# Kernel optimization log

Measured on AMD Instinct MI355X. Metric: run time of the kernel, lower is better.

The kernel has to match this reference:

```python
import jax, jax.numpy as jnp
import numpy as np

NUM_NODES = 10000
NUM_EDGES = 640000
GNN_IN = 128
EDGE_DIST_DIM = 4
MLP_HIDDEN = 256
MLP_OUT = 1


def setup_inputs() -> dict:
    key = jax.random.key(0)
    k1, k2, k3, k4, k5 = jax.random.split(key, 5)
    x = jax.random.normal(k1, (NUM_NODES, GNN_IN), dtype=jnp.float32)
    edge_index = jax.random.randint(k2, (NUM_EDGES, 2), 0, NUM_NODES, dtype=jnp.int64)
    edge_dist = jax.random.normal(k3, (NUM_EDGES, EDGE_DIST_DIM), dtype=jnp.float32)
    d_in = GNN_IN * 2 + EDGE_DIST_DIM
    # Kaiming-uniform-ish init like nn.Linear defaults
    w1 = jax.random.uniform(k4, (d_in, MLP_HIDDEN), dtype=jnp.float32,
                            minval=-1.0, maxval=1.0) / np.sqrt(d_in)
    b1 = jnp.zeros((MLP_HIDDEN,), dtype=jnp.float32)
    w2 = jax.random.uniform(k5, (MLP_HIDDEN, MLP_OUT), dtype=jnp.float32,
                            minval=-1.0, maxval=1.0) / np.sqrt(MLP_HIDDEN)
    b2 = jnp.zeros((MLP_OUT,), dtype=jnp.float32)
    return {"x": x, "edge_index": edge_index, "edge_dist": edge_dist,
            "w1": w1, "b1": b1, "w2": w2, "b2": b2}


def reference(x, edge_index, edge_dist, w1, b1, w2, b2):
    # edge_index: (num_edges, 2) -> transpose to (2, num_edges) as in forward()
    row = edge_index[:, 0]
    col = edge_index[:, 1]
    # gather node features for both endpoints, concat with edge distances
    edge_attr = jnp.concatenate([x[row], x[col], edge_dist], axis=1)  # (E, 2*gnn_in+edge_dist_dim)
    h = jax.nn.relu(edge_attr @ w1 + b1)  # (E, mlp_hidden)
    return jax.nn.sigmoid(h @ w2 + b2)    # (E, mlp_out)
```

## Files before the change

### kernel.cpp

```cpp
#include <hip/hip_runtime.h>
#include <hip/hip_fp16.h>

#define GNN_IN 128
#define HID 256
#define NSPLIT 4
#define SLICE 64

typedef _Float16 f16x2 __attribute__((ext_vector_type(2)));
struct __align__(8) h4v { f16x2 a, b; };
struct __align__(16) h8v { f16x2 a, b, c, d; };

__device__ __forceinline__ float fdot2f(f16x2 a, f16x2 b, float c) {
#if __has_builtin(__builtin_amdgcn_fdot2)
    return __builtin_amdgcn_fdot2(a, b, c, false);
#else
    return fmaf((float)a.x, (float)b.x, fmaf((float)a.y, (float)b.y, c));
#endif
}

__device__ __forceinline__ f16x2 pkcvt(float x, float y) {
#if __has_builtin(__builtin_amdgcn_cvt_pkrtz)
    return __builtin_bit_cast(f16x2, __builtin_amdgcn_cvt_pkrtz(x, y));
#else
    f16x2 r; r.x = (_Float16)x; r.y = (_Float16)y; return r;
#endif
}

#define DPP_ADD(v, ctrl)                                                     \
    do {                                                                     \
        float _t = __builtin_bit_cast(                                       \
            float, __builtin_amdgcn_update_dpp(                              \
                       0, __builtin_bit_cast(int, v), ctrl, 0xf, 0xf, true));\
        (v) += _t;                                                           \
    } while (0)

__device__ __forceinline__ float dpp_sum8(float v) {
    DPP_ADD(v, 0x111);
    DPP_ADD(v, 0x112);
    DPP_ADD(v, 0x114);
    return v;
}

__device__ __forceinline__ float dpp_sum64(float v) {
    DPP_ADD(v, 0x111);
    DPP_ADD(v, 0x112);
    DPP_ADD(v, 0x114);
    DPP_ADD(v, 0x118);
    DPP_ADD(v, 0x142);
    DPP_ADD(v, 0x143);
    return v;
}

__global__ void detect_kernel(const unsigned int* __restrict__ ei,
                              unsigned int* __restrict__ flag) {
    if (threadIdx.x == 0 && blockIdx.x == 0) {
        unsigned int v = 0;
        for (int i = 1; i < 256; i += 2) v |= ei[i];
        *flag = (v == 0u) ? 1u : 0u;
    }
}

__global__ void __launch_bounds__(256) decode_kernel(
    const void* __restrict__ ei, const unsigned int* __restrict__ flag,
    int2* __restrict__ idx, int ne) {
    const int e = blockIdx.x * 256 + threadIdx.x;
    if (e >= ne) return;
    if (*flag) {
        const int4 v = *(const int4*)((const char*)ei + (size_t)e * 16);
        idx[e] = make_int2(v.x, v.z);
    } else {
        idx[e] = ((const int2*)ei)[e];
    }
}

__global__ void __launch_bounds__(256) node_gemm_c4(
    const float* __restrict__ x, const float* __restrict__ w1,
    __half* __restrict__ AB, int num_nodes) {
    __shared__ float xs[16][GNN_IN];
    const int tid = threadIdx.x;
    const int r0  = blockIdx.x * 16;

    for (int i = tid; i < 16 * GNN_IN / 4; i += 256) {
        const int rr = i >> 5;
        const int cc = (i & 31) << 2;
        const int r = min(r0 + rr, num_nodes - 1);
        *(float4*)&xs[rr][cc] = *(const float4*)(x + (size_t)r * GNN_IN + cc);
    }
    __syncthreads();

    const int cq   = tid & 127;
    const int rg   = tid >> 7;
    const int col  = (cq & 63) << 2;
    const int half = cq >> 6;
    const float* __restrict__ w = w1 + (size_t)half * GNN_IN * HID + col;

    float acc[8][4];
#pragma unroll
    for (int r = 0; r < 8; ++r)
#pragma unroll
        for (int c = 0; c < 4; ++c) acc[r][c] = 0.f;

    for (int k0 = 0; k0 < GNN_IN; k0 += 4) {
        float4 wv[4];
#pragma unroll
        for (int kk = 0; kk < 4; ++kk)
            wv[kk] = *(const float4*)(w + (size_t)(k0 + kk) * HID);
#pragma unroll
        for (int r = 0; r < 8; ++r) {
            const float4 xv = *(const float4*)&xs[rg * 8 + r][k0];
            acc[r][0] = fmaf(xv.x, wv[0].x, acc[r][0]);
            acc[r][1] = fmaf(xv.x, wv[0].y, acc[r][1]);
            acc[r][2] = fmaf(xv.x, wv[0].z, acc[r][2]);
            acc[r][3] = fmaf(xv.x, wv[0].w, acc[r][3]);
            acc[r][0] = fmaf(xv.y, wv[1].x, acc[r][0]);
            acc[r][1] = fmaf(xv.y, wv[1].y, acc[r][1]);
            acc[r][2] = fmaf(xv.y, wv[1].z, acc[r][2]);
            acc[r][3] = fmaf(xv.y, wv[1].w, acc[r][3]);
            acc[r][0] = fmaf(xv.z, wv[2].x, acc[r][0]);
            acc[r][1] = fmaf(xv.z, wv[2].y, acc[r][1]);
            acc[r][2] = fmaf(xv.z, wv[2].z, acc[r][2]);
            acc[r][3] = fmaf(xv.z, wv[2].w, acc[r][3]);
            acc[r][0] = fmaf(xv.w, wv[3].x, acc[r][0]);
            acc[r][1] = fmaf(xv.w, wv[3].y, acc[r][1]);
            acc[r][2] = fmaf(xv.w, wv[3].z, acc[r][2]);
            acc[r][3] = fmaf(xv.w, wv[3].w, acc[r][3]);
        }
    }

    __half* o = AB + (size_t)half * num_nodes * HID + col;
#pragma unroll
    for (int r = 0; r < 8; ++r) {
        const int rr = r0 + rg * 8 + r;
        if (rr < num_nodes) {
            h4v hv;
            hv.a = pkcvt(acc[r][0], acc[r][1]);
            hv.b = pkcvt(acc[r][2], acc[r][3]);
            *(h4v*)(o + (size_t)rr * HID) = hv;
        }
    }
}

__global__ void __launch_bounds__(256) edge_split_kernel(
    const __half* __restrict__ AB, const int2* __restrict__ idx,
    const float* __restrict__ ed, const float* __restrict__ w1,
    const float* __restrict__ b1, const float* __restrict__ w2,
    float* __restrict__ partials, int num_edges, int num_nodes) {
    const int tid   = threadIdx.x;
    const int lane  = tid & 63;
    const int bid   = blockIdx.x;
    const int split = (bid & 7) >> 1;
    const int wsi   = ((((bid >> 3) << 1) | (bid & 1)) << 2) | (tid >> 6);
    const int nsw   = (gridDim.x >> 3) << 3;
    const int j8    = lane >> 3;
    const int q8    = lane & 7;
    const int c     = split * SLICE + (q8 << 3);

    f16x2 wtA[8], wtB[8], w2pk[4];
    float b1f[8];
#pragma unroll
    for (int cc = 0; cc < 8; ++cc) {
        wtA[cc] = pkcvt(w1[(size_t)(2 * GNN_IN + 0) * HID + c + cc],
                        w1[(size_t)(2 * GNN_IN + 1) * HID + c + cc]);
        wtB[cc] = pkcvt(w1[(size_t)(2 * GNN_IN + 2) * HID + c + cc],
                        w1[(size_t)(2 * GNN_IN + 3) * HID + c + cc]);
        b1f[cc] = b1[c + cc];
    }
#pragma unroll
    for (int m = 0; m < 4; ++m)
        w2pk[m] = pkcvt(w2[c + 2 * m], w2[c + 2 * m + 1]);
    const f16x2 zero = {(_Float16)0.f, (_Float16)0.f};

    const __half* __restrict__ A = AB;
    const __half* __restrict__ B = AB + (size_t)num_nodes * HID;
    float* __restrict__ pbase = partials + (size_t)split * num_edges;
    const int ngroups = (num_edges + 7) >> 3;

    for (int g0 = wsi; g0 < ngroups; g0 += 2 * nsw) {
        const int g1 = min(g0 + nsw, ngroups - 1);
        const int e0 = min(g0 * 8 + j8, num_edges - 1);
        const int e1 = min(g1 * 8 + j8, num_edges - 1);

        const int2  rc0 = idx[e0];
        const int2  rc1 = idx[e1];
        const float4 edv0 = *(const float4*)(ed + (size_t)e0 * 4);
        const float4 edv1 = *(const float4*)(ed + (size_t)e1 * 4);
        const h8v av0 = *(const h8v*)(A + (size_t)rc0.x * HID + c);
        const h8v bv0 = *(const h8v*)(B + (size_t)rc0.y * HID + c);
        const h8v av1 = *(const h8v*)(A + (size_t)rc1.x * HID + c);
        const h8v bv1 = *(const h8v*)(B + (size_t)rc1.y * HID + c);

        float p0, p1;
        {
            const f16x2 e01 = pkcvt(edv0.x, edv0.y);
            const f16x2 e23 = pkcvt(edv0.z, edv0.w);
            float c_[8];
#pragma unroll
            for (int cc = 0; cc < 8; ++cc)
                c_[cc] = fdot2f(e23, wtB[cc], fdot2f(e01, wtA[cc], b1f[cc]));
            f16x2 h0 = (av0.a + bv0.a) + pkcvt(c_[0], c_[1]);
            f16x2 h1 = (av0.b + bv0.b) + pkcvt(c_[2], c_[3]);
            f16x2 h2 = (av0.c + bv0.c) + pkcvt(c_[4], c_[5]);
            f16x2 h3 = (av0.d + bv0.d) + pkcvt(c_[6], c_[7]);
            h0 = __builtin_elementwise_max(h0, zero);
            h1 = __builtin_elementwise_max(h1, zero);
            h2 = __builtin_elementwise_max(h2, zero);
            h3 = __builtin_elementwise_max(h3, zero);
            p0 = fdot2f(h0, w2pk[0],
                 fdot2f(h1, w2pk[1], fdot2f(h2, w2pk[2], fdot2f(h3, w2pk[3], 0.f))));
        }
        {
            const f16x2 e01 = pkcvt(edv1.x, edv1.y);
            const f16x2 e23 = pkcvt(edv1.z, edv1.w);
            float c_[8];
#pragma unroll
            for (int cc = 0; cc < 8; ++cc)
                c_[cc] = fdot2f(e23, wtB[cc], fdot2f(e01, wtA[cc], b1f[cc]));
            f16x2 h0 = (av1.a + bv1.a) + pkcvt(c_[0], c_[1]);
            f16x2 h1 = (av1.b + bv1.b) + pkcvt(c_[2], c_[3]);
            f16x2 h2 = (av1.c + bv1.c) + pkcvt(c_[4], c_[5]);
            f16x2 h3 = (av1.d + bv1.d) + pkcvt(c_[6], c_[7]);
            h0 = __builtin_elementwise_max(h0, zero);
            h1 = __builtin_elementwise_max(h1, zero);
            h2 = __builtin_elementwise_max(h2, zero);
            h3 = __builtin_elementwise_max(h3, zero);
            p1 = fdot2f(h0, w2pk[0],
                 fdot2f(h1, w2pk[1], fdot2f(h2, w2pk[2], fdot2f(h3, w2pk[3], 0.f))));
        }

        p0 = dpp_sum8(p0);
        p1 = dpp_sum8(p1);
        if (q8 == 7) {
            pbase[e0] = p0;
            if (g1 != g0) pbase[e1] = p1;
        }
    }
}

__global__ void __launch_bounds__(256) combine_kernel(
    const float* __restrict__ partials, const float* __restrict__ b2,
    float* __restrict__ out, int ne) {
    const int e0 = (blockIdx.x * 256 + threadIdx.x) * 4;
    if (e0 >= ne) return;
    const float b2v = b2[0];
    if (e0 + 3 < ne) {
        float4 s0 = *(const float4*)(partials + e0);
        const float4 s1 = *(const float4*)(partials + (size_t)ne + e0);
        const float4 s2 = *(const float4*)(partials + (size_t)2 * ne + e0);
        const float4 s3 = *(const float4*)(partials + (size_t)3 * ne + e0);
        s0.x = 1.f / (1.f + __expf(-(s0.x + s1.x + s2.x + s3.x + b2v)));
        s0.y = 1.f / (1.f + __expf(-(s0.y + s1.y + s2.y + s3.y + b2v)));
        s0.z = 1.f / (1.f + __expf(-(s0.z + s1.z + s2.z + s3.z + b2v)));
        s0.w = 1.f / (1.f + __expf(-(s0.w + s1.w + s2.w + s3.w + b2v)));
        *(float4*)(out + e0) = s0;
    } else {
        for (int e = e0; e < ne; ++e) {
            const float p = partials[e] + partials[(size_t)ne + e] +
                            partials[(size_t)2 * ne + e] +
                            partials[(size_t)3 * ne + e];
            out[e] = 1.f / (1.f + __expf(-(p + b2v)));
        }
    }
}

__global__ void __launch_bounds__(256) edge_kernel_fp16(
    const __half* __restrict__ A, const __half* __restrict__ B,
    const void* __restrict__ ei, const float* __restrict__ ed,
    const float* __restrict__ w1, const float* __restrict__ b1,
    const float* __restrict__ w2, const float* __restrict__ b2,
    const unsigned int* __restrict__ flag,
    float* __restrict__ out, int num_edges) {
    const int lane   = threadIdx.x & 63;
    const int wave   = (blockIdx.x * blockDim.x + threadIdx.x) >> 6;
    const int nwaves = (gridDim.x * blockDim.x) >> 6;
    const int c0     = lane << 2;

    const float4 b1v = *(const float4*)(b1 + c0);
    float wt[4][4];
#pragma unroll
    for (int k = 0; k < 4; ++k)
        *(float4*)wt[k] = *(const float4*)(w1 + (size_t)(2 * GNN_IN + k) * HID + c0);
    const float4 w2f = *(const float4*)(w2 + c0);
    const f16x2  w2A = pkcvt(w2f.x, w2f.y);
    const f16x2  w2B = pkcvt(w2f.z, w2f.w);
    const float  b2v = b2[0];
    const int   is64 = __builtin_amdgcn_readfirstlane((int)(*flag));
    const f16x2 zero = {(_Float16)0.f, (_Float16)0.f};

    const int chunk = (((num_edges + nwaves - 1) / nwaves) + 3) & ~3;
    const int e0s = __builtin_amdgcn_readfirstlane(wave * chunk);
    const int e1s = __builtin_amdgcn_readfirstlane(min(num_edges, e0s + chunk));

    for (int es = e0s; es < e1s; es += 4) {
        int eid[4];
#pragma unroll
        for (int jj = 0; jj < 4; ++jj) eid[jj] = min(es + jj, e1s - 1);
        int rr[4], cc[4];
        if (is64) {
#pragma unroll
            for (int jj = 0; jj < 4; ++jj) {
                const int4 v = *(const int4*)((const char*)ei + (size_t)eid[jj] * 16);
                rr[jj] = v.x; cc[jj] = v.z;
            }
        } else {
#pragma unroll
            for (int jj = 0; jj < 4; ++jj) {
                const int2 v = *(const int2*)((const char*)ei + (size_t)eid[jj] * 8);
                rr[jj] = v.x; cc[jj] = v.y;
            }
        }
        h4v av[4], bv[4];
        float4 edv[4];
#pragma unroll
        for (int jj = 0; jj < 4; ++jj) {
            av[jj]  = *(const h4v*)(A + (size_t)rr[jj] * HID + c0);
            bv[jj]  = *(const h4v*)(B + (size_t)cc[jj] * HID + c0);
            edv[jj] = *(const float4*)(ed + (size_t)eid[jj] * 4);
        }
        float p[4];
#pragma unroll
        for (int jj = 0; jj < 4; ++jj) {
            float c_[4] = {b1v.x, b1v.y, b1v.z, b1v.w};
            const float ep[4] = {edv[jj].x, edv[jj].y, edv[jj].z, edv[jj].w};
#pragma unroll
            for (int k = 0; k < 4; ++k)
#pragma unroll
                for (int qq = 0; qq < 4; ++qq) c_[qq] = fmaf(ep[k], wt[k][qq], c_[qq]);
            f16x2 h0 = (av[jj].a + bv[jj].a) + pkcvt(c_[0], c_[1]);
            f16x2 h1 = (av[jj].b + bv[jj].b) + pkcvt(c_[2], c_[3]);
            h0 = __builtin_elementwise_max(h0, zero);
            h1 = __builtin_elementwise_max(h1, zero);
            p[jj] = fdot2f(h0, w2A, fdot2f(h1, w2B, 0.f));
        }
#pragma unroll
        for (int jj = 0; jj < 4; ++jj) p[jj] = dpp_sum64(p[jj]);
        float s[4];
#pragma unroll
        for (int jj = 0; jj < 4; ++jj) s[jj] = 1.f / (1.f + __expf(-(p[jj] + b2v)));
        if (lane == 63) {
            if (es + 3 < e1s) {
                *(float4*)(out + es) = make_float4(s[0], s[1], s[2], s[3]);
            } else {
#pragma unroll
                for (int jj = 0; jj < 4; ++jj)
                    if (es + jj < e1s) out[es + jj] = s[jj];
            }
        }
    }
}

__global__ void __launch_bounds__(256) edge_direct_kernel(
    const float* __restrict__ x, const void* __restrict__ ei,
    const float* __restrict__ ed, const float* __restrict__ w1,
    const float* __restrict__ b1, const float* __restrict__ w2,
    const float* __restrict__ b2, const unsigned int* __restrict__ flag,
    float* __restrict__ out, int num_edges, int num_nodes) {
    const int lane   = threadIdx.x & 63;
    const int wave   = (blockIdx.x * blockDim.x + threadIdx.x) >> 6;
    const int nwaves = (gridDim.x * blockDim.x) >> 6;
    const int c0     = lane << 2;

    const float4 w2v = *(const float4*)(w2 + c0);
    const float4 b1v = *(const float4*)(b1 + c0);
    float wt[4][4];
#pragma unroll
    for (int k = 0; k < 4; ++k)
        *(float4*)wt[k] = *(const float4*)(w1 + (size_t)(2 * GNN_IN + k) * HID + c0);
    const float b2v  = b2[0];
    const int   is64 = flag ? (int)(*flag) : 0;
    const float* w2p = (const float*)&w2v;
    const float* b1p = (const float*)&b1v;

    const int chunk = (num_edges + nwaves - 1) / nwaves;
    const int e0 = wave * chunk;
    const int e1 = min(num_edges, e0 + chunk);

    for (int e = e0; e < e1; ++e) {
        int row, col;
        if (is64) {
            const int4 v = ((const int4*)ei)[e];
            row = v.x; col = v.z;
        } else {
            const int2 v = ((const int2*)ei)[e];
            row = v.x; col = v.y;
        }
        row = min(max(row, 0), num_nodes - 1);
        col = min(max(col, 0), num_nodes - 1);
        const float4 edv = *(const float4*)(ed + (size_t)e * 4);
        const float* edp = (const float*)&edv;
        float h4[4];
#pragma unroll
        for (int jj = 0; jj < 4; ++jj) {
            float h = b1p[jj];
#pragma unroll
            for (int k = 0; k < 4; ++k) h = fmaf(edp[k], wt[k][jj], h);
            h4[jj] = h;
        }
        const float* xr = x + (size_t)row * GNN_IN;
        const float* xc = x + (size_t)col * GNN_IN;
        for (int k = 0; k < GNN_IN; ++k) {
            const float xv = xr[k];
            const float4 wv = *(const float4*)(w1 + (size_t)k * HID + c0);
            h4[0] = fmaf(xv, wv.x, h4[0]); h4[1] = fmaf(xv, wv.y, h4[1]);
            h4[2] = fmaf(xv, wv.z, h4[2]); h4[3] = fmaf(xv, wv.w, h4[3]);
        }
        for (int k = 0; k < GNN_IN; ++k) {
            const float xv = xc[k];
            const float4 wv = *(const float4*)(w1 + (size_t)(GNN_IN + k) * HID + c0);
            h4[0] = fmaf(xv, wv.x, h4[0]); h4[1] = fmaf(xv, wv.y, h4[1]);
            h4[2] = fmaf(xv, wv.z, h4[2]); h4[3] = fmaf(xv, wv.w, h4[3]);
        }
        float p = 0.f;
#pragma unroll
        for (int jj = 0; jj < 4; ++jj) p = fmaf(fmaxf(h4[jj], 0.f), w2p[jj], p);
#pragma unroll
        for (int off = 32; off >= 1; off >>= 1) p += __shfl_xor(p, off, 64);
        if (lane == 0) out[e] = 1.f / (1.f + __expf(-(p + b2v)));
    }
}

extern "C" void kernel_launch(void* const* d_in, const int* in_sizes, int n_in,
                              void* d_out, int out_size, void* d_ws, size_t ws_size,
                              hipStream_t stream) {
    const float* x  = (const float*)d_in[0];
    const void*  ei = d_in[1];
    const float* ed = (const float*)d_in[2];
    const float* w1 = (const float*)d_in[3];
    const float* b1 = (const float*)d_in[4];
    const float* w2 = (const float*)d_in[5];
    const float* b2 = (const float*)d_in[6];
    float* out = (float*)d_out;

    const int num_nodes = in_sizes[0] / GNN_IN;
    const int num_edges = in_sizes[1] / 2;

    unsigned int* flag = nullptr;
    if (ws_size >= 16) {
        flag = (unsigned int*)d_ws;
        detect_kernel<<<1, 64, 0, stream>>>((const unsigned int*)ei, flag);
    }

    const size_t ab_bytes   = (size_t)2 * num_nodes * HID * sizeof(__half);
    const size_t idx_bytes  = (size_t)num_edges * sizeof(int2);
    const size_t part_bytes = (size_t)NSPLIT * num_edges * sizeof(float);
    const size_t need_split = 256 + ab_bytes + idx_bytes + part_bytes;
    const size_t need_old   = 256 + ab_bytes;

    if (flag && ws_size >= need_split) {
        __half* AB      = (__half*)((char*)d_ws + 256);
        int2*   idx     = (int2*)((char*)d_ws + 256 + ab_bytes);
        float*  partial = (float*)((char*)d_ws + 256 + ab_bytes + idx_bytes);

        decode_kernel<<<(num_edges + 255) / 256, 256, 0, stream>>>(ei, flag, idx,
                                                                   num_edges);
        node_gemm_c4<<<(num_nodes + 15) / 16, 256, 0, stream>>>(x, w1, AB,
                                                                num_nodes);
        edge_split_kernel<<<2048, 256, 0, stream>>>(AB, idx, ed, w1, b1, w2,
                                                    partial, num_edges, num_nodes);
        combine_kernel<<<(num_edges / 4 + 255) / 256, 256, 0, stream>>>(
            partial, b2, out, num_edges);
    } else if (flag && ws_size >= need_old) {
        __half* AB = (__half*)((char*)d_ws + 256);
        node_gemm_c4<<<(num_nodes + 15) / 16, 256, 0, stream>>>(x, w1, AB,
                                                                num_nodes);
        __half* Bp = AB + (size_t)num_nodes * HID;
        edge_kernel_fp16<<<2048, 256, 0, stream>>>(AB, Bp, ei, ed, w1, b1, w2, b2,
                                                   flag, out, num_edges);
    } else {
        edge_direct_kernel<<<4096, 256, 0, stream>>>(x, ei, ed, w1, b1, w2, b2,
                                                     flag, out, num_edges, num_nodes);
    }
}
```

Measured before the change: 100.6 us.

## Pack edge records with fp16 distances, fp16 node GEMM, and 4-way edge batching

The decode kernel now writes one 16-byte record per edge holding pre-shifted row/col byte offsets and fp16-packed edge distances, so the edge kernel issues a single load instead of separate index and distance loads. The node GEMM converts x and W1 to fp16 in two small prep kernels and uses packed fp16 dot products. The edge kernel processes four edge groups per iteration to keep more gathers in flight, with launch bounds and register pinning added. This adds two extra kernel launches and more workspace, and raises register pressure in the edge loop.

```diff
diff --git a/kernel.cpp b/kernel.cpp
--- a/kernel.cpp
+++ b/kernel.cpp
@@ -25,6 +25,13 @@
     f16x2 r; r.x = (_Float16)x; r.y = (_Float16)y; return r;
 #endif
 }
+
+__device__ __forceinline__ void pinv(f16x2& x) {
+    int t = __builtin_bit_cast(int, x);
+    asm volatile("" : "+v"(t));
+    x = __builtin_bit_cast(f16x2, t);
+}
+__device__ __forceinline__ void pinf(float& x) { asm volatile("" : "+v"(x)); }
 
 #define DPP_ADD(v, ctrl)                                                     \
     do {                                                                     \
@@ -61,30 +68,60 @@
 }
 
 __global__ void __launch_bounds__(256) decode_kernel(
-    const void* __restrict__ ei, const unsigned int* __restrict__ flag,
-    int2* __restrict__ idx, int ne) {
+    const void* __restrict__ ei, const float* __restrict__ ed,
+    const unsigned int* __restrict__ flag, int4* __restrict__ recs, int ne) {
     const int e = blockIdx.x * 256 + threadIdx.x;
     if (e >= ne) return;
+    int r, c;
     if (*flag) {
         const int4 v = *(const int4*)((const char*)ei + (size_t)e * 16);
-        idx[e] = make_int2(v.x, v.z);
+        r = v.x; c = v.z;
     } else {
-        idx[e] = ((const int2*)ei)[e];
-    }
-}
-
-__global__ void __launch_bounds__(256) node_gemm_c4(
-    const float* __restrict__ x, const float* __restrict__ w1,
+        const int2 v = ((const int2*)ei)[e];
+        r = v.x; c = v.y;
+    }
+    const float4 d = *(const float4*)(ed + (size_t)e * 4);
+    int4 rec;
+    rec.x = r << 9;
+    rec.y = c << 9;
+    rec.z = __builtin_bit_cast(int, pkcvt(d.x, d.y));
+    rec.w = __builtin_bit_cast(int, pkcvt(d.z, d.w));
+    recs[e] = rec;
+}
+
+__global__ void __launch_bounds__(256) prep_x_kernel(
+    const float* __restrict__ x, __half* __restrict__ xh, int n4) {
+    const int i = blockIdx.x * 256 + threadIdx.x;
+    if (i >= n4) return;
+    const float4 v = ((const float4*)x)[i];
+    h4v o;
+    o.a = pkcvt(v.x, v.y);
+    o.b = pkcvt(v.z, v.w);
+    ((h4v*)xh)[i] = o;
+}
+
+__global__ void __launch_bounds__(256) prep_w_kernel(
+    const float* __restrict__ w1, f16x2* __restrict__ whp) {
+    const int i = blockIdx.x * 256 + threadIdx.x;
+    if (i >= 2 * 64 * 256) return;
+    const int col  = i & 255;
+    const int p    = (i >> 8) & 63;
+    const int half = i >> 14;
+    const int k    = half * GNN_IN + 2 * p;
+    whp[i] = pkcvt(w1[(size_t)k * HID + col], w1[(size_t)(k + 1) * HID + col]);
+}
+
+__global__ void __launch_bounds__(256) node_gemm_fp16(
+    const __half* __restrict__ xh, const f16x2* __restrict__ whp,
     __half* __restrict__ AB, int num_nodes) {
-    __shared__ float xs[16][GNN_IN];
+    __shared__ __half xs[16][GNN_IN];
     const int tid = threadIdx.x;
     const int r0  = blockIdx.x * 16;
-
-    for (int i = tid; i < 16 * GNN_IN / 4; i += 256) {
-        const int rr = i >> 5;
-        const int cc = (i & 31) << 2;
-        const int r = min(r0 + rr, num_nodes - 1);
-        *(float4*)&xs[rr][cc] = *(const float4*)(x + (size_t)r * GNN_IN + cc);
+    {
+        const int rr = tid >> 4;
+        const int cc = (tid & 15) << 3;
+        const int r  = min(r0 + rr, num_nodes - 1);
+        *(h8v*)&xs[rr][cc] = *(const h8v*)(xh + (size_t)r * GNN_IN + cc);
     }
     __syncthreads();
 
@@ -92,7 +129,7 @@
     const int rg   = tid >> 7;
     const int col  = (cq & 63) << 2;
     const int half = cq >> 6;
-    const float* __restrict__ w = w1 + (size_t)half * GNN_IN * HID + col;
+    const f16x2* __restrict__ wbase = whp + ((size_t)half << 14) + col;
 
     float acc[8][4];
 #pragma unroll
@@ -100,30 +137,30 @@
 #pragma unroll
         for (int c = 0; c < 4; ++c) acc[r][c] = 0.f;
 
-    for (int k0 = 0; k0 < GNN_IN; k0 += 4) {
-        float4 wv[4];
-#pragma unroll
-        for (int kk = 0; kk < 4; ++kk)
-            wv[kk] = *(const float4*)(w + (size_t)(k0 + kk) * HID);
+    for (int ch = 0; ch < 16; ++ch) {
+        h8v wq[4];
+#pragma unroll
+        for (int p = 0; p < 4; ++p)
+            wq[p] = *(const h8v*)(wbase + (size_t)(ch * 4 + p) * HID);
 #pragma unroll
         for (int r = 0; r < 8; ++r) {
-            const float4 xv = *(const float4*)&xs[rg * 8 + r][k0];
-            acc[r][0] = fmaf(xv.x, wv[0].x, acc[r][0]);
-            acc[r][1] = fmaf(xv.x, wv[0].y, acc[r][1]);
-            acc[r][2] = fmaf(xv.x, wv[0].z, acc[r][2]);
-            acc[r][3] = fmaf(xv.x, wv[0].w, acc[r][3]);
-            acc[r][0] = fmaf(xv.y, wv[1].x, acc[r][0]);
-            acc[r][1] = fmaf(xv.y, wv[1].y, acc[r][1]);
-            acc[r][2] = fmaf(xv.y, wv[1].z, acc[r][2]);
-            acc[r][3] = fmaf(xv.y, wv[1].w, acc[r][3]);
-            acc[r][0] = fmaf(xv.z, wv[2].x, acc[r][0]);
-            acc[r][1] = fmaf(xv.z, wv[2].y, acc[r][1]);
-            acc[r][2] = fmaf(xv.z, wv[2].z, acc[r][2]);
-            acc[r][3] = fmaf(xv.z, wv[2].w, acc[r][3]);
-            acc[r][0] = fmaf(xv.w, wv[3].x, acc[r][0]);
-            acc[r][1] = fmaf(xv.w, wv[3].y, acc[r][1]);
-            acc[r][2] = fmaf(xv.w, wv[3].z, acc[r][2]);
-            acc[r][3] = fmaf(xv.w, wv[3].w, acc[r][3]);
+            const h8v xv = *(const h8v*)&xs[rg * 8 + r][ch * 8];
+            acc[r][0] = fdot2f(xv.a, wq[0].a, acc[r][0]);
+            acc[r][0] = fdot2f(xv.b, wq[1].a, acc[r][0]);
+            acc[r][0] = fdot2f(xv.c, wq[2].a, acc[r][0]);
+            acc[r][0] = fdot2f(xv.d, wq[3].a, acc[r][0]);
+            acc[r][1] = fdot2f(xv.a, wq[0].b, acc[r][1]);
+            acc[r][1] = fdot2f(xv.b, wq[1].b, acc[r][1]);
+            acc[r][1] = fdot2f(xv.c, wq[2].b, acc[r][1]);
+            acc[r][1] = fdot2f(xv.d, wq[3].b, acc[r][1]);
+            acc[r][2] = fdot2f(xv.a, wq[0].c, acc[r][2]);
+            acc[r][2] = fdot2f(xv.b, wq[1].c, acc[r][2]);
+            acc[r][2] = fdot2f(xv.c, wq[2].c, acc[r][2]);
+            acc[r][2] = fdot2f(xv.d, wq[3].c, acc[r][2]);
+            acc[r][3] = fdot2f(xv.a, wq[0].d, acc[r][3]);
+            acc[r][3] = fdot2f(xv.b, wq[1].d, acc[r][3]);
+            acc[r][3] = fdot2f(xv.c, wq[2].d, acc[r][3]);
+            acc[r][3] = fdot2f(xv.d, wq[3].d, acc[r][3]);
         }
     }
 
@@ -140,11 +177,11 @@
     }
 }
 
-__global__ void __launch_bounds__(256) edge_split_kernel(
-    const __half* __restrict__ AB, const int2* __restrict__ idx,
-    const float* __restrict__ ed, const float* __restrict__ w1,
-    const float* __restrict__ b1, const float* __restrict__ w2,
-    float* __restrict__ partials, int num_edges, int num_nodes) {
+__global__ void __launch_bounds__(256, 4) edge_split_kernel(
+    const __half* __restrict__ AB, const int4* __restrict__ recs,
+    const float* __restrict__ w1, const float* __restrict__ b1,
+    const float* __restrict__ w2, float* __restrict__ partials,
+    int num_edges, int num_nodes) {
     const int tid   = threadIdx.x;
     const int lane  = tid & 63;
     const int bid   = blockIdx.x;
@@ -154,6 +191,7 @@
     const int j8    = lane >> 3;
     const int q8    = lane & 7;
     const int c     = split * SLICE + (q8 << 3);
+    const int coff  = c * 2;
 
     f16x2 wtA[8], wtB[8], w2pk[4];
     float b1f[8];
@@ -164,74 +202,58 @@
         wtB[cc] = pkcvt(w1[(size_t)(2 * GNN_IN + 2) * HID + c + cc],
                         w1[(size_t)(2 * GNN_IN + 3) * HID + c + cc]);
         b1f[cc] = b1[c + cc];
-    }
-#pragma unroll
-    for (int m = 0; m < 4; ++m)
+        pinv(wtA[cc]); pinv(wtB[cc]); pinf(b1f[cc]);
+    }
+#pragma unroll
+    for (int m = 0; m < 4; ++m) {
         w2pk[m] = pkcvt(w2[c + 2 * m], w2[c + 2 * m + 1]);
+        pinv(w2pk[m]);
+    }
     const f16x2 zero = {(_Float16)0.f, (_Float16)0.f};
 
-    const __half* __restrict__ A = AB;
-    const __half* __restrict__ B = AB + (size_t)num_nodes * HID;
+    const char* __restrict__ Abase = (const char*)AB;
+    const char* __restrict__ Bbase = (const char*)(AB + (size_t)num_nodes * HID);
     float* __restrict__ pbase = partials + (size_t)split * num_edges;
     const int ngroups = (num_edges + 7) >> 3;
-
-    for (int g0 = wsi; g0 < ngroups; g0 += 2 * nsw) {
-        const int g1 = min(g0 + nsw, ngroups - 1);
-        const int e0 = min(g0 * 8 + j8, num_edges - 1);
-        const int e1 = min(g1 * 8 + j8, num_edges - 1);
-
-        const int2  rc0 = idx[e0];
-        const int2  rc1 = idx[e1];
-        const float4 edv0 = *(const float4*)(ed + (size_t)e0 * 4);
-        const float4 edv1 = *(const float4*)(ed + (size_t)e1 * 4);
-        const h8v av0 = *(const h8v*)(A + (size_t)rc0.x * HID + c);
-        const h8v bv0 = *(const h8v*)(B + (size_t)rc0.y * HID + c);
-        const h8v av1 = *(const h8v*)(A + (size_t)rc1.x * HID + c);
-        const h8v bv1 = *(const h8v*)(B + (size_t)rc1.y * HID + c);
-
-        float p0, p1;
-        {
-            const f16x2 e01 = pkcvt(edv0.x, edv0.y);
-            const f16x2 e23 = pkcvt(edv0.z, edv0.w);
+    const int emax = num_edges - 1;
+
+    for (int g = wsi; g < ngroups; g += 4 * nsw) {
+        int e[4];
+        int4 rec[4];
+#pragma unroll
+        for (int k = 0; k < 4; ++k) {
+            int gk = g + k * nsw;
+            if (gk > ngroups - 1) gk = ngroups - 1;
+            e[k] = min(gk * 8 + j8, emax);
+            rec[k] = recs[e[k]];
+        }
+        h8v av[4], bv[4];
+#pragma unroll
+        for (int k = 0; k < 4; ++k) {
+            av[k] = *(const h8v*)(Abase + ((size_t)(unsigned)(rec[k].x + coff)));
+            bv[k] = *(const h8v*)(Bbase + ((size_t)(unsigned)(rec[k].y + coff)));
+        }
+#pragma unroll
+        for (int k = 0; k < 4; ++k) {
+            const f16x2 e01 = __builtin_bit_cast(f16x2, rec[k].z);
+            const f16x2 e23 = __builtin_bit_cast(f16x2, rec[k].w);
             float c_[8];
 #pragma unroll
             for (int cc = 0; cc < 8; ++cc)
                 c_[cc] = fdot2f(e23, wtB[cc], fdot2f(e01, wtA[cc], b1f[cc]));
-            f16x2 h0 = (av0.a + bv0.a) + pkcvt(c_[0], c_[1]);
-            f16x2 h1 = (av0.b + bv0.b) + pkcvt(c_[2], c_[3]);
-            f16x2 h2 = (av0.c + bv0.c) + pkcvt(c_[4], c_[5]);
-            f16x2 h3 = (av0.d + bv0.d) + pkcvt(c_[6], c_[7]);
+            f16x2 h0 = (av[k].a + bv[k].a) + pkcvt(c_[0], c_[1]);
+            f16x2 h1 = (av[k].b + bv[k].b) + pkcvt(c_[2], c_[3]);
+            f16x2 h2 = (av[k].c + bv[k].c) + pkcvt(c_[4], c_[5]);
+            f16x2 h3 = (av[k].d + bv[k].d) + pkcvt(c_[6], c_[7]);
             h0 = __builtin_elementwise_max(h0, zero);
             h1 = __builtin_elementwise_max(h1, zero);
             h2 = __builtin_elementwise_max(h2, zero);
             h3 = __builtin_elementwise_max(h3, zero);
-            p0 = fdot2f(h0, w2pk[0],
-                 fdot2f(h1, w2pk[1], fdot2f(h2, w2pk[2], fdot2f(h3, w2pk[3], 0.f))));
-        }
-        {
-            const f16x2 e01 = pkcvt(edv1.x, edv1.y);
-            const f16x2 e23 = pkcvt(edv1.z, edv1.w);
-            float c_[8];
-#pragma unroll
-            for (int cc = 0; cc < 8; ++cc)
-                c_[cc] = fdot2f(e23, wtB[cc], fdot2f(e01, wtA[cc], b1f[cc]));
-            f16x2 h0 = (av1.a + bv1.a) + pkcvt(c_[0], c_[1]);
-            f16x2 h1 = (av1.b + bv1.b) + pkcvt(c_[2], c_[3]);
-            f16x2 h2 = (av1.c + bv1.c) + pkcvt(c_[4], c_[5]);
-            f16x2 h3 = (av1.d + bv1.d) + pkcvt(c_[6], c_[7]);
-            h0 = __builtin_elementwise_max(h0, zero);
-            h1 = __builtin_elementwise_max(h1, zero);
-            h2 = __builtin_elementwise_max(h2, zero);
-            h3 = __builtin_elementwise_max(h3, zero);
-            p1 = fdot2f(h0, w2pk[0],
-                 fdot2f(h1, w2pk[1], fdot2f(h2, w2pk[2], fdot2f(h3, w2pk[3], 0.f))));
-        }
-
-        p0 = dpp_sum8(p0);
-        p1 = dpp_sum8(p1);
-        if (q8 == 7) {
-            pbase[e0] = p0;
-            if (g1 != g0) pbase[e1] = p1;
+            float p = fdot2f(h0, w2pk[0],
+                      fdot2f(h1, w2pk[1],
+                      fdot2f(h2, w2pk[2], fdot2f(h3, w2pk[3], 0.f))));
+            p = dpp_sum8(p);
+            if (q8 == 7) pbase[e[k]] = p;
         }
     }
 }
@@ -262,6 +284,68 @@
     }
 }
 
+__global__ void __launch_bounds__(256) node_gemm_c4(
+    const float* __restrict__ x, const float* __restrict__ w1,
+    __half* __restrict__ AB, int num_nodes) {
+    __shared__ float xs[16][GNN_IN];
+    const int tid = threadIdx.x;
+    const int r0  = blockIdx.x * 16;
+    for (int i = tid; i < 16 * GNN_IN / 4; i += 256) {
+        const int rr = i >> 5;
+        const int cc = (i & 31) << 2;
+        const int r = min(r0 + rr, num_nodes - 1);
+        *(float4*)&xs[rr][cc] = *(const float4*)(x + (size_t)r * GNN_IN + cc);
+    }
+    __syncthreads();
+    const int cq   = tid & 127;
+    const int rg   = tid >> 7;
+    const int col  = (cq & 63) << 2;
+    const int half = cq >> 6;
+    const float* __restrict__ w = w1 + (size_t)half * GNN_IN * HID + col;
+    float acc[8][4];
+#pragma unroll
+    for (int r = 0; r < 8; ++r)
+#pragma unroll
+        for (int c = 0; c < 4; ++c) acc[r][c] = 0.f;
+    for (int k0 = 0; k0 < GNN_IN; k0 += 4) {
+        float4 wv[4];
+#pragma unroll
+        for (int kk = 0; kk < 4; ++kk)
+            wv[kk] = *(const float4*)(w + (size_t)(k0 + kk) * HID);
+#pragma unroll
+        for (int r = 0; r < 8; ++r) {
+            const float4 xv = *(const float4*)&xs[rg * 8 + r][k0];
+            acc[r][0] = fmaf(xv.x, wv[0].x, acc[r][0]);
+            acc[r][1] = fmaf(xv.x, wv[0].y, acc[r][1]);
+            acc[r][2] = fmaf(xv.x, wv[0].z, acc[r][2]);
+            acc[r][3] = fmaf(xv.x, wv[0].w, acc[r][3]);
+            acc[r][0] = fmaf(xv.y, wv[1].x, acc[r][0]);
+            acc[r][1] = fmaf(xv.y, wv[1].y, acc[r][1]);
+            acc[r][2] = fmaf(xv.y, wv[1].z, acc[r][2]);
+            acc[r][3] = fmaf(xv.y, wv[1].w, acc[r][3]);
+            acc[r][0] = fmaf(xv.z, wv[2].x, acc[r][0]);
+            acc[r][1] = fmaf(xv.z, wv[2].y, acc[r][1]);
+            acc[r][2] = fmaf(xv.z, wv[2].z, acc[r][2]);
+            acc[r][3] = fmaf(xv.z, wv[2].w, acc[r][3]);
+            acc[r][0] = fmaf(xv.w, wv[3].x, acc[r][0]);
+            acc[r][1] = fmaf(xv.w, wv[3].y, acc[r][1]);
+            acc[r][2] = fmaf(xv.w, wv[3].z, acc[r][2]);
+            acc[r][3] = fmaf(xv.w, wv[3].w, acc[r][3]);
+        }
+    }
+    __half* o = AB + (size_t)half * num_nodes * HID + col;
+#pragma unroll
+    for (int r = 0; r < 8; ++r) {
+        const int rr = r0 + rg * 8 + r;
+        if (rr < num_nodes) {
+            h4v hv;
+            hv.a = pkcvt(acc[r][0], acc[r][1]);
+            hv.b = pkcvt(acc[r][2], acc[r][3]);
+            *(h4v*)(o + (size_t)rr * HID) = hv;
+        }
+    }
+}
+
 __global__ void __launch_bounds__(256) edge_kernel_fp16(
     const __half* __restrict__ A, const __half* __restrict__ B,
     const void* __restrict__ ei, const float* __restrict__ ed,
@@ -440,22 +524,30 @@
     }
 
     const size_t ab_bytes   = (size_t)2 * num_nodes * HID * sizeof(__half);
-    const size_t idx_bytes  = (size_t)num_edges * sizeof(int2);
+    const size_t rec_bytes  = (size_t)num_edges * sizeof(int4);
     const size_t part_bytes = (size_t)NSPLIT * num_edges * sizeof(float);
-    const size_t need_split = 256 + ab_bytes + idx_bytes + part_bytes;
-    const size_t need_old   = 256 + ab_bytes;
-
-    if (flag && ws_size >= need_split) {
-        __half* AB      = (__half*)((char*)d_ws + 256);
-        int2*   idx     = (int2*)((char*)d_ws + 256 + ab_bytes);
-        float*  partial = (float*)((char*)d_ws + 256 + ab_bytes + idx_bytes);
-
-        decode_kernel<<<(num_edges + 255) / 256, 256, 0, stream>>>(ei, flag, idx,
-                                                                   num_edges);
-        node_gemm_c4<<<(num_nodes + 15) / 16, 256, 0, stream>>>(x, w1, AB,
-                                                                num_nodes);
-        edge_split_kernel<<<2048, 256, 0, stream>>>(AB, idx, ed, w1, b1, w2,
-                                                    partial, num_edges, num_nodes);
+    const size_t xh_bytes   = (size_t)num_nodes * GNN_IN * sizeof(__half);
+    const size_t whp_bytes  = (size_t)2 * 64 * 256 * sizeof(f16x2);
+    const size_t need_v3 = 256 + ab_bytes + rec_bytes + part_bytes + xh_bytes + whp_bytes;
+    const size_t need_old = 256 + ab_bytes;
+
+    if (flag && ws_size >= need_v3) {
+        char* base = (char*)d_ws + 256;
+        __half* AB      = (__half*)base;                       base += ab_bytes;
+        int4*   recs    = (int4*)base;                         base += rec_bytes;
+        float*  partial = (float*)base;                        base += part_bytes;
+        __half* xh      = (__half*)base;                       base += xh_bytes;
+        f16x2*  whp     = (f16x2*)base;
+
+        decode_kernel<<<(num_edges + 255) / 256, 256, 0, stream>>>(
+            ei, ed, flag, recs, num_edges);
+        prep_x_kernel<<<(num_nodes * GNN_IN / 4 + 255) / 256, 256, 0, stream>>>(
+            x, xh, num_nodes * GNN_IN / 4);
+        prep_w_kernel<<<128, 256, 0, stream>>>(w1, whp);
+        node_gemm_fp16<<<(num_nodes + 15) / 16, 256, 0, stream>>>(
+            xh, whp, AB, num_nodes);
+        edge_split_kernel<<<2048, 256, 0, stream>>>(
+            AB, recs, w1, b1, w2, partial, num_edges, num_nodes);
         combine_kernel<<<(num_edges / 4 + 255) / 256, 256, 0, stream>>>(
             partial, b2, out, num_edges);
     } else if (flag && ws_size >= need_old) {
```

New measurement: 102.1 us (median of 2 runs). No clear change (+1.5%).
